# Kernel tuning notes

Hardware: AMD Instinct MI355X
Metric: run time of the kernel (lower is better)

## Reference

```python
import jax, jax.numpy as jnp
import numpy as np

B, L, C, S, W, R = 2, 32, 32, 64, 64, 32
MH = 32  # forcing MLP hidden


def _conv3d(x, w, b, pad_hw):
    # x: [B, Cin, L, S, W], w: [Cout, Cin, 1, kh, kw]
    y = jax.lax.conv_general_dilated(
        x, w, window_strides=(1, 1, 1),
        padding=[(0, 0), (pad_hw, pad_hw), (pad_hw, pad_hw)],
        dimension_numbers=('NCDHW', 'OIDHW', 'NCDHW'))
    return y + b[None, :, None, None, None]


def _forward(x, listT, params_log_base, dispersion_mod, fm_W1, fm_b1, fm_W2, fm_b2,
             forcing_scale, U_re, U_im, V_re, V_im, pW_re, pW_im, pb_re, pb_im,
             convr_w, convr_b, convi_w, convi_b, projc_w, projc_b, ln_w, ln_b):
    b, l, c, s, w = x.shape
    r = U_re.shape[-1]
    pad = s // 4
    dt = listT.reshape(b, l, 1, 1, 1)

    # FFT with mirror padding along S
    xp = jnp.pad(x, ((0, 0), (0, 0), (0, 0), (pad, pad), (0, 0)), mode='reflect')
    h = jnp.fft.fft2(xp.astype(jnp.complex64), axes=(-2, -1), norm='ortho')

    # complex channel projection
    proj_W = pW_re + 1j * pW_im
    h = jnp.einsum('blcsw,cd->bldsw', h, proj_W)
    h = h + (pb_re + 1j * pb_im)[None, None, :, None, None]

    # back to spatial, crop pad, re-FFT
    hs = jnp.fft.ifft2(h, axes=(-2, -1), norm='ortho')[..., pad:-pad, :]
    h = jnp.fft.fft2(hs, axes=(-2, -1), norm='ortho')

    U = U_re + 1j * U_im          # [C, S, R]
    V = V_re + 1j * V_im          # [C, W, R]
    # zq[b,l,c,r,q] = sum_{s,w} h * conj(U)[c,s,r] * V[c,w,q]
    zq = jnp.einsum('blcsw,csr,cwq->blcrq', h, jnp.conj(U), V)

    nu_base = jnp.exp(params_log_base[0] + dispersion_mod[0]).reshape(1, 1, c, r, 1)
    th_base = jnp.exp(params_log_base[1] + dispersion_mod[1]).reshape(1, 1, c, r, 1)

    # forcing modulation
    ctx = x.mean(axis=(-2, -1))                       # [B, L, C]
    inp = jnp.concatenate([ctx, dt.reshape(b, l, 1)], axis=-1)
    mid = jnp.tanh(inp @ fm_W1 + fm_b1)
    mod = (mid @ fm_W2 + fm_b2).reshape(b, l, c, r, 2)
    dnu = (forcing_scale * jnp.tanh(mod[..., 0]))[..., None]
    dth = (forcing_scale * jnp.tanh(mod[..., 1]))[..., None]

    nu_t = jnp.maximum(nu_base * dt + dnu, 1e-6)       # [B, L, C, R, 1]
    th_t = th_base * dt + dth
    lamb = jnp.exp(jax.lax.complex(-nu_t, th_t))       # complex [B, L, C, R, 1]

    gamma = jnp.sqrt(jnp.maximum(1.0 - jnp.exp(-2.0 * nu_t), 1e-12))
    x_in = zq * gamma.astype(zq.dtype)                 # [B, L, C, R, R]

    # parallel linear-recurrence scan: z_t = lamb_t * z_{t-1} + x_t
    def comb(a, bb):
        a1, x1 = a
        a2, x2 = bb
        return a1 * a2, a2 * x1 + x2
    _, z_out = jax.lax.associative_scan(comb, (lamb, x_in), axis=1)

    # reconstruct spectral field and inverse FFT
    h_rec = jnp.einsum('blcrq,cwq,csr->blcsw', z_out, jnp.conj(V), U)
    h_sp = jnp.fft.ifft2(h_rec, axes=(-2, -1), norm='ortho')

    xr = jnp.transpose(h_sp.real, (0, 2, 1, 3, 4))     # [B, C, L, S, W]
    xi = jnp.transpose(h_sp.imag, (0, 2, 1, 3, 4))
    hr = _conv3d(xr, convr_w, convr_b, 1)
    hi = _conv3d(xi, convi_w, convi_b, 1)
    hf = _conv3d(jnp.concatenate([hr, hi], axis=1), projc_w, projc_b, 0)
    hf = jnp.transpose(hf, (0, 2, 1, 3, 4))            # [B, L, C, S, W]

    # LayerNorm over [S, W]
    mu = hf.mean(axis=(-2, -1), keepdims=True)
    var = hf.var(axis=(-2, -1), keepdims=True)
    hf = (hf - mu) / jnp.sqrt(var + 1e-5) * ln_w + ln_b

    return x + hf


def setup_inputs() -> dict:
    key = jax.random.key(0)
    ks = jax.random.split(key, 20)
    f32 = jnp.float32
    x = jax.random.normal(ks[0], (B, L, C, S, W), dtype=f32)
    listT = jax.random.uniform(ks[1], (B, L), dtype=f32, minval=0.5, maxval=1.5)

    r_min, r_max = 0.8, 0.99
    u1 = jax.random.uniform(ks[2], (C, R), dtype=f32)
    u2 = jax.random.uniform(ks[3], (C, R), dtype=f32)
    nu_log = jnp.log(-0.5 * jnp.log(u1 * (r_max ** 2 - r_min ** 2) + r_min ** 2))
    theta_log = jnp.log(u2 * (2.0 * np.pi))
    params_log_base = jnp.stack([nu_log, theta_log], axis=0)
    dispersion_mod = jnp.zeros((2, C, R), dtype=f32)

    fm_W1 = jax.random.normal(ks[4], (C + 1, MH), dtype=f32) / np.sqrt(C + 1)
    fm_b1 = jnp.zeros((MH,), dtype=f32)
    fm_W2 = jax.random.normal(ks[5], (MH, C * R * 2), dtype=f32) / np.sqrt(MH)
    fm_b2 = jnp.zeros((C * R * 2,), dtype=f32)
    forcing_scale = jnp.float32(0.1)

    cplx_scale = 1.0 / np.sqrt(2.0)
    U_re = jax.random.normal(ks[6], (C, S, R), dtype=f32) * cplx_scale / np.sqrt(S)
    U_im = jax.random.normal(ks[7], (C, S, R), dtype=f32) * cplx_scale / np.sqrt(S)
    V_re = jax.random.normal(ks[8], (C, W, R), dtype=f32) * cplx_scale / np.sqrt(W)
    V_im = jax.random.normal(ks[9], (C, W, R), dtype=f32) * cplx_scale / np.sqrt(W)
    pW_re = jax.random.normal(ks[10], (C, C), dtype=f32) * cplx_scale / np.sqrt(C)
    pW_im = jax.random.normal(ks[11], (C, C), dtype=f32) * cplx_scale / np.sqrt(C)
    pb_re = jnp.zeros((C,), dtype=f32)
    pb_im = jnp.zeros((C,), dtype=f32)

    convr_w = jax.random.normal(ks[12], (C, C, 1, 3, 3), dtype=f32) * (1.0 / np.sqrt(C * 9))
    convr_b = jnp.zeros((C,), dtype=f32)
    convi_w = jax.random.normal(ks[13], (C, C, 1, 3, 3), dtype=f32) * (1.0 / np.sqrt(C * 9))
    convi_b = jnp.zeros((C,), dtype=f32)
    projc_w = jax.random.normal(ks[14], (C, 2 * C, 1, 1, 1), dtype=f32) * (1.0 / np.sqrt(2 * C))
    projc_b = jnp.zeros((C,), dtype=f32)

    ln_w = jnp.ones((S, W), dtype=f32)
    ln_b = jnp.zeros((S, W), dtype=f32)

    return dict(x=x, listT=listT, params_log_base=params_log_base,
                dispersion_mod=dispersion_mod, fm_W1=fm_W1, fm_b1=fm_b1,
                fm_W2=fm_W2, fm_b2=fm_b2, forcing_scale=forcing_scale,
                U_re=U_re, U_im=U_im, V_re=V_re, V_im=V_im,
                pW_re=pW_re, pW_im=pW_im, pb_re=pb_re, pb_im=pb_im,
                convr_w=convr_w, convr_b=convr_b, convi_w=convi_w, convi_b=convi_b,
                projc_w=projc_w, projc_b=projc_b, ln_w=ln_w, ln_b=ln_b)


def reference(x, listT, params_log_base, dispersion_mod, fm_W1, fm_b1, fm_W2, fm_b2,
              forcing_scale, U_re, U_im, V_re, V_im, pW_re, pW_im, pb_re, pb_im,
              convr_w, convr_b, convi_w, convi_b, projc_w, projc_b, ln_w, ln_b):
    return _forward(x, listT, params_log_base, dispersion_mod, fm_W1, fm_b1, fm_W2,
                    fm_b2, forcing_scale, U_re, U_im, V_re, V_im, pW_re, pW_im,
                    pb_re, pb_im, convr_w, convr_b, convi_w, convi_b, projc_w,
                    projc_b, ln_w, ln_b)
```

## Files before the change

kernel.cpp:

```cpp
#include <hip/hip_runtime.h>


typedef __attribute__((ext_vector_type(8))) short short8;
typedef __attribute__((ext_vector_type(4))) float floatx4;

__device__ __forceinline__ unsigned pack_bf16(float re, float im) {
  unsigned a = __float_as_uint(re), b = __float_as_uint(im);
  a = (a + 0x7FFFu + ((a >> 16) & 1u)) >> 16;
  b = (b + 0x7FFFu + ((b >> 16) & 1u)) >> 16;
  return a | (b << 16);
}
__device__ __forceinline__ unsigned short bf16r(float v) {
  unsigned a = __float_as_uint(v);
  return (unsigned short)((a + 0x7FFFu + ((a >> 16) & 1u)) >> 16);
}

__global__ __launch_bounds__(256) void k_mixprep(
    const float* __restrict__ x, const float* __restrict__ pWr,
    const float* __restrict__ pWi,
    const float* __restrict__ U_re, const float* __restrict__ U_im,
    const float* __restrict__ V_re, const float* __restrict__ V_im,
    const float* __restrict__ projc_w, const float* __restrict__ convr_w,
    const float* __restrict__ convi_w,
    const float* __restrict__ listT, const float* __restrict__ plb,
    const float* __restrict__ dmod, const float* __restrict__ W1,
    const float* __restrict__ b1, const float* __restrict__ W2,
    const float* __restrict__ b2, const float* __restrict__ fscale,
    unsigned* __restrict__ hs, unsigned* __restrict__ zqA,
    unsigned* __restrict__ recA, unsigned* __restrict__ recB,
    unsigned* __restrict__ Wtb, float2* __restrict__ lam,
    float* __restrict__ gam) {
  __shared__ __align__(16) char smem[33280];
  const int tid = threadIdx.x;
  const int bid = blockIdx.x;
  if (bid < 64) {
    float* cred = (float*)smem;
    float* ctxs = cred + 256;
    float* mid_s = ctxs + 32;
    const int bl = bid;
    {
      int c = tid >> 3, sub = tid & 7;
      const float4* xb = (const float4*)(x + (size_t)bl * 131072 + c * 4096);
      float s = 0.f;
#pragma unroll 8
      for (int m = 0; m < 128; ++m) {
        float4 v = xb[sub + m * 8];
        s += v.x + v.y + v.z + v.w;
      }
      cred[c * 8 + sub] = s;
    }
    __syncthreads();
    if (tid < 32) {
      float t = 0.f;
#pragma unroll
      for (int k = 0; k < 8; ++k) t += cred[tid * 8 + k];
      ctxs[tid] = t * (1.f / 4096.f);
    }
    __syncthreads();
    float dt = listT[bl];
    if (tid < 32) {
      float a = b1[tid];
      for (int j = 0; j < 32; ++j) a += ctxs[j] * W1[j * 32 + tid];
      a += dt * W1[1024 + tid];
      mid_s[tid] = tanhf(a);
    }
    __syncthreads();
    float fs = fscale[0];
#pragma unroll
    for (int u = 0; u < 4; ++u) {
      int cr = u * 256 + tid;
      int col = cr * 2;
      float m0 = b2[col], m1 = b2[col + 1];
      for (int h = 0; h < 32; ++h) {
        float mh = mid_s[h];
        float2 w2 = *(const float2*)&W2[h * 2048 + col];
        m0 += mh * w2.x;
        m1 += mh * w2.y;
      }
      float dnu = fs * tanhf(m0);
      float dth = fs * tanhf(m1);
      float nub = expf(plb[cr] + dmod[cr]);
      float thb = expf(plb[1024 + cr] + dmod[1024 + cr]);
      float nut = fmaxf(nub * dt + dnu, 1e-6f);
      float tht = thb * dt + dth;
      float e = expf(-nut);
      float sa, ca;
      sincosf(tht, &sa, &ca);
      float g = sqrtf(fmaxf(1.f - expf(-2.f * nut), 1e-12f));
      int o = bl * 1024 + cr;
      lam[o] = make_float2(e * ca, e * sa);
      gam[o] = g;
    }
  } else if (bid < 1088) {
    unsigned* xb_s = (unsigned*)smem;
    unsigned* outb = (unsigned*)smem;
    const int wk = bid - 64;
    const int bl = wk >> 4;
    const int seg = wk & 15;
    const int pxbase = seg * 256;
    const float* xb = x + (size_t)bl * 131072 + pxbase;
#pragma unroll
    for (int t = 0; t < 4; ++t) {
      int i = t * 256 + tid;
      int c2 = i & 15, g4 = i >> 4;
      float4 a = *(const float4*)(xb + (2 * c2) * 4096 + g4 * 4);
      float4 b = *(const float4*)(xb + (2 * c2 + 1) * 4096 + g4 * 4);
#pragma unroll
      for (int j = 0; j < 4; ++j) {
        int px = g4 * 4 + j;
        xb_s[px * 20 + (((c2 >> 2) ^ (px & 3)) << 2) + (c2 & 3)] =
            pack_bf16(((const float*)&a)[j], ((const float*)&b)[j]);
      }
    }
    const int lane = tid & 63, wv = tid >> 6;
    const int qd = lane >> 4, ln = lane & 15;
    short8 arL, aiL, arH, aiH;
#pragma unroll
    for (int j = 0; j < 8; ++j) {
      int ci = qd * 8 + j;
      ((short*)&arL)[j] = (short)bf16r(pWr[ci * 32 + ln]);
      ((short*)&aiL)[j] = (short)bf16r(pWi[ci * 32 + ln]);
      ((short*)&arH)[j] = (short)bf16r(pWr[ci * 32 + 16 + ln]);
      ((short*)&aiH)[j] = (short)bf16r(pWi[ci * 32 + 16 + ln]);
    }
    __syncthreads();
    floatx4 RL[4], IL[4], RH[4], IH[4];
#pragma unroll
    for (int pt = 0; pt < 4; ++pt) {
      int pxt = wv * 4 + pt;
      int pxl = pxt * 16 + ln;
      short8 bfr = *(const short8*)&xb_s[pxl * 20 + ((qd ^ (pxl & 3)) << 2)];
      floatx4 z4 = {0.f, 0.f, 0.f, 0.f};
      RL[pt] = __builtin_amdgcn_mfma_f32_16x16x32_bf16(arL, bfr, z4, 0, 0, 0);
      IL[pt] = __builtin_amdgcn_mfma_f32_16x16x32_bf16(aiL, bfr, z4, 0, 0, 0);
      RH[pt] = __builtin_amdgcn_mfma_f32_16x16x32_bf16(arH, bfr, z4, 0, 0, 0);
      IH[pt] = __builtin_amdgcn_mfma_f32_16x16x32_bf16(aiH, bfr, z4, 0, 0, 0);
    }
    __syncthreads();
#pragma unroll
    for (int pt = 0; pt < 4; ++pt) {
      int px = (wv * 4 + pt) * 16 + ln;
#pragma unroll
      for (int j = 0; j < 4; ++j) {
        outb[(qd * 4 + j) * 260 + px] = pack_bf16(RL[pt][j], IL[pt][j]);
        outb[(16 + qd * 4 + j) * 260 + px] = pack_bf16(RH[pt][j], IH[pt][j]);
      }
    }
    __syncthreads();
    unsigned* ho = hs + (size_t)bl * 131072 + pxbase;
    const int px4 = tid & 63, dg = tid >> 6;
#pragma unroll
    for (int dd = 0; dd < 8; ++dd) {
      int d = dg * 8 + dd;
      uint4 v = *(const uint4*)&outb[d * 260 + px4 * 4];
      *(uint4*)(ho + d * 4096 + px4 * 4) = v;
    }
  } else if (bid < 1152) {
    float2* A2 = (float2*)smem;
    float2* tw = (float2*)(smem + 16384);
    const int id = bid - 1088;
    const int c = id >> 1, src = id & 1;
    const float* Ar = (src ? V_re : U_re) + c * 2048;
    const float* Ai = (src ? V_im : U_im) + c * 2048;
    if (tid < 64) {
      float sa, ca;
      sincosf((float)tid * 0.09817477042468103f, &sa, &ca);
      tw[tid] = make_float2(ca, sa);
    }
#pragma unroll
    for (int t = 0; t < 8; ++t) {
      int idx = t * 256 + tid;
      A2[idx] = make_float2(Ar[idx], Ai[idx]);
    }
    __syncthreads();
    const int kw = tid >> 2, mg = tid & 3;
    float sr[8] = {0.f, 0.f, 0.f, 0.f, 0.f, 0.f, 0.f, 0.f};
    float si[8] = {0.f, 0.f, 0.f, 0.f, 0.f, 0.f, 0.f, 0.f};
#pragma unroll 4
    for (int n = 0; n < 64; ++n) {
      float2 w = tw[(kw * n) & 63];
      float ws = src ? -w.y : w.y;
#pragma unroll
      for (int t4 = 0; t4 < 4; ++t4) {
        float4 q = *(const float4*)&A2[n * 32 + mg * 8 + t4 * 2];
        sr[2 * t4]     += q.x * w.x - q.y * ws;
        si[2 * t4]     += q.x * ws + q.y * w.x;
        sr[2 * t4 + 1] += q.z * w.x - q.w * ws;
        si[2 * t4 + 1] += q.z * ws + q.w * w.x;
      }
    }
#pragma unroll
    for (int j = 0; j < 8; ++j) {
      float r = sr[j] * 0.125f, i2 = si[j] * 0.125f;
      int m = mg * 8 + j;
      unsigned p_ri  = pack_bf16(r, i2);
      unsigned p_rmi = pack_bf16(r, -i2);
      unsigned p_ir  = pack_bf16(i2, r);
      unsigned p_mir = pack_bf16(-i2, r);
      if (src == 0) {
        zqA[((c * 4 + 2) * 32 + m) * 64 + kw] = p_ri;
        zqA[((c * 4 + 3) * 32 + m) * 64 + kw] = p_mir;
        recA[((c * 2 + 0) * 64 + kw) * 32 + m] = p_rmi;
        recA[((c * 2 + 1) * 64 + kw) * 32 + m] = p_ir;
      } else {
        zqA[((c * 4 + 0) * 32 + m) * 64 + kw] = p_rmi;
        zqA[((c * 4 + 1) * 32 + m) * 64 + kw] = p_ir;
        recB[((c * 2 + 0) * 64 + kw) * 32 + m] = p_ri;
        recB[((c * 2 + 1) * 64 + kw) * 32 + m] = p_mir;
      }
    }
  } else {
    int gid = (bid - 1152) * 256 + tid;
    if (gid < 9216) {
      int co = gid / 288;
      int r2 = gid - co * 288;
      int tap = r2 >> 5, ci = r2 & 31;
      float sr = 0.f, si = 0.f;
      for (int m = 0; m < 32; ++m) {
        sr += projc_w[co * 64 + m]      * convr_w[(m * 32 + ci) * 9 + tap];
        si += projc_w[co * 64 + 32 + m] * convi_w[(m * 32 + ci) * 9 + tap];
      }
      Wtb[gid] = pack_bf16(sr, si);
    }
  }
}

__global__ __launch_bounds__(512, 2) void k_mid(
    const unsigned* __restrict__ hs, const short* __restrict__ zqA,
    const short* __restrict__ recA, const short* __restrict__ recB,
    const float2* __restrict__ lam, const float* __restrict__ gam,
    unsigned* __restrict__ hsp) {
  __shared__ __align__(16) char smem[61440];
  float2* lam_s = (float2*)smem;
  float*  gam_s = (float*)(smem + 8192);
  unsigned* HsB = (unsigned*)(smem + 12288);
  float2* zqt   = (float2*)(smem + 12288);
  unsigned* zB  = (unsigned*)(smem + 28672);
  unsigned* T2P = (unsigned*)(smem + 45056);
  const int tid = threadIdx.x;
  const int b = blockIdx.x >> 5, c = blockIdx.x & 31;
  const int lane = tid & 63, wv = tid >> 6;
  const int grp = wv >> 2, wvg = wv & 3;
  const int tg = tid & 255;
  const int qd = lane >> 4, ln = lane & 15;
  const int mt = wvg >> 1, nth = wvg & 1;
  const short* zA = zqA + (size_t)c * 4 * 32 * 128;
  short8 a1[4], a2[4], a3[4], a4[4];
#pragma unroll
  for (int t = 0; t < 4; ++t) {
    int row = mt * 16 + ln;
    a1[t] = *(const short8*)(zA + (0 * 32 + row) * 128 + t * 32 + qd * 8);
    a2[t] = *(const short8*)(zA + (1 * 32 + row) * 128 + t * 32 + qd * 8);
    a3[t] = *(const short8*)(zA + (2 * 32 + row) * 128 + t * 32 + qd * 8);
    a4[t] = *(const short8*)(zA + (3 * 32 + row) * 128 + t * 32 + qd * 8);
  }
  const short* rA = recA + (size_t)c * 2 * 64 * 64;
  short8 a5[2], a6[2];
#pragma unroll
  for (int t = 0; t < 2; ++t) {
    int row = wvg * 16 + ln;
    a5[t] = *(const short8*)(rA + (0 * 64 + row) * 64 + t * 32 + qd * 8);
    a6[t] = *(const short8*)(rA + (1 * 64 + row) * 64 + t * 32 + qd * 8);
  }
  const short* rB = recB + (size_t)c * 2 * 64 * 64;
  for (int idx = tid; idx < 1024; idx += 512) {
    int l = idx >> 5, r = idx & 31;
    lam_s[idx] = lam[(b * 32 + l) * 1024 + c * 32 + r];
    gam_s[idx] = gam[(b * 32 + l) * 1024 + c * 32 + r];
  }
  {
    const uint4* hp =
        (const uint4*)(hs + (size_t)((b * 32 + grp) * 32 + c) * 4096);
#pragma unroll
    for (int it = 0; it < 4; ++it) {
      int i4 = tg + it * 256;
      uint4 v = hp[i4];
      int s = i4 >> 4, w4 = i4 & 15;
      *(uint4*)&HsB[grp * 4096 + s * 64 + ((w4 ^ (s & 15)) << 2)] = v;
    }
  }
  float2 st[4];
#pragma unroll
  for (int j = 0; j < 4; ++j) st[j] = make_float2(0.f, 0.f);
  __syncthreads();
  for (int round = 0; round < 16; ++round) {
    const int l0 = round * 2;
    const int blc = (b * 32 + l0 + grp) * 32 + c;
#pragma unroll
    for (int nti = 0; nti < 2; ++nti) {
      int nt = nth * 2 + nti;
      int n = nt * 16 + ln;
      floatx4 accr = {0.f, 0.f, 0.f, 0.f}, acci = {0.f, 0.f, 0.f, 0.f};
#pragma unroll
      for (int t = 0; t < 4; ++t) {
        short8 bb = *(const short8*)&HsB[grp * 4096 + n * 64 +
                                         (((4 * t + qd) ^ (n & 15)) << 2)];
        accr = __builtin_amdgcn_mfma_f32_16x16x32_bf16(a1[t], bb, accr, 0, 0, 0);
        acci = __builtin_amdgcn_mfma_f32_16x16x32_bf16(a2[t], bb, acci, 0, 0, 0);
      }
#pragma unroll
      for (int j = 0; j < 4; ++j) {
        int q = mt * 16 + qd * 4 + j;
        int s = n;
        T2P[grp * 2048 + q * 64 + (((s >> 2) ^ (q & 15)) << 2) + (s & 3)] =
            pack_bf16(accr[j], acci[j]);
      }
    }
    __syncthreads();
    {
      int n = nth * 16 + ln;
      floatx4 zr = {0.f, 0.f, 0.f, 0.f}, zi = {0.f, 0.f, 0.f, 0.f};
#pragma unroll
      for (int t = 0; t < 4; ++t) {
        short8 bb = *(const short8*)&T2P[grp * 2048 + n * 64 +
                                         (((4 * t + qd) ^ (n & 15)) << 2)];
        zr = __builtin_amdgcn_mfma_f32_16x16x32_bf16(a3[t], bb, zr, 0, 0, 0);
        zi = __builtin_amdgcn_mfma_f32_16x16x32_bf16(a4[t], bb, zi, 0, 0, 0);
      }
#pragma unroll
      for (int j = 0; j < 4; ++j) {
        int r = mt * 16 + qd * 4 + j;
        zqt[grp * 1024 + r * 32 + n] = make_float2(zr[j], zi[j]);
      }
    }
    __syncthreads();
    {
      int q = nth * 16 + ln;
#pragma unroll
      for (int j = 0; j < 4; ++j) {
        int r = mt * 16 + qd * 4 + j;
        float2 lm = lam_s[l0 * 32 + r];
        float g = gam_s[l0 * 32 + r];
        float2 v = zqt[r * 32 + q];
        float nr = lm.x * st[j].x - lm.y * st[j].y + g * v.x;
        float ni = lm.x * st[j].y + lm.y * st[j].x + g * v.y;
        st[j] = make_float2(nr, ni);
        unsigned pk = pack_bf16(nr, ni);
        lm = lam_s[(l0 + 1) * 32 + r];
        g = gam_s[(l0 + 1) * 32 + r];
        v = zqt[1024 + r * 32 + q];
        nr = lm.x * st[j].x - lm.y * st[j].y + g * v.x;
        ni = lm.x * st[j].y + lm.y * st[j].x + g * v.y;
        st[j] = make_float2(nr, ni);
        if (grp) pk = pack_bf16(nr, ni);
        zB[grp * 1024 + q * 32 + (((r >> 2) ^ (q & 7)) << 2) + (r & 3)] = pk;
      }
    }
    __syncthreads();
#pragma unroll
    for (int nt = 0; nt < 2; ++nt) {
      int n = nt * 16 + ln;
      floatx4 pr = {0.f, 0.f, 0.f, 0.f}, pi = {0.f, 0.f, 0.f, 0.f};
#pragma unroll
      for (int t = 0; t < 2; ++t) {
        short8 bb = *(const short8*)&zB[grp * 1024 + n * 32 +
                                        (((4 * t + qd) ^ (n & 7)) << 2)];
        pr = __builtin_amdgcn_mfma_f32_16x16x32_bf16(a5[t], bb, pr, 0, 0, 0);
        pi = __builtin_amdgcn_mfma_f32_16x16x32_bf16(a6[t], bb, pi, 0, 0, 0);
      }
#pragma unroll
      for (int j = 0; j < 4; ++j) {
        int s = wvg * 16 + qd * 4 + j;
        int q = n;
        T2P[grp * 2048 + s * 32 + (((q >> 2) ^ (s & 7)) << 2) + (q & 3)] =
            pack_bf16(pr[j], pi[j]);
      }
    }
    __syncthreads();
    uint4 sv[4];
    const bool more = (round < 15);
    if (more) {
      const uint4* hp = (const uint4*)(
          hs + (size_t)((b * 32 + l0 + 2 + grp) * 32 + c) * 4096);
#pragma unroll
      for (int it = 0; it < 4; ++it) sv[it] = hp[tg + it * 256];
    }
    {
      short8 pa[2];
      int row = wvg * 16 + ln;
#pragma unroll
      for (int t = 0; t < 2; ++t)
        pa[t] = *(const short8*)&T2P[grp * 2048 + row * 32 +
                                     (((4 * t + qd) ^ (row & 7)) << 2)];
      unsigned* ho = hsp + (size_t)blc * 4096;
#pragma unroll
      for (int nt = 0; nt < 4; ++nt) {
        int n = nt * 16 + ln;
        floatx4 hr = {0.f, 0.f, 0.f, 0.f}, hi = {0.f, 0.f, 0.f, 0.f};
#pragma unroll
        for (int t = 0; t < 2; ++t) {
          short8 b5 = *(const short8*)(rB + (0 * 64 + n) * 64 + t * 32 + qd * 8);
          short8 b6 = *(const short8*)(rB + (1 * 64 + n) * 64 + t * 32 + qd * 8);
          hr = __builtin_amdgcn_mfma_f32_16x16x32_bf16(pa[t], b5, hr, 0, 0, 0);
          hi = __builtin_amdgcn_mfma_f32_16x16x32_bf16(pa[t], b6, hi, 0, 0, 0);
        }
#pragma unroll
        for (int j = 0; j < 4; ++j) {
          int s = wvg * 16 + qd * 4 + j;
          ho[s * 64 + n] = pack_bf16(hr[j], hi[j]);
        }
      }
    }
    if (more) {
#pragma unroll
      for (int it = 0; it < 4; ++it) {
        int i4 = tg + it * 256;
        int s = i4 >> 4, w4 = i4 & 15;
        *(uint4*)&HsB[grp * 4096 + s * 64 + ((w4 ^ (s & 15)) << 2)] = sv[it];
      }
    }
    __syncthreads();
  }
}

__global__ __launch_bounds__(256, 2) void k_conv(
    const unsigned* __restrict__ hsp, const short* __restrict__ Wtb,
    unsigned short* __restrict__ convout, float2* __restrict__ stats) {
  __shared__ unsigned lds_in[6 * 66 * 32];
  const int bl = blockIdx.x >> 4;
  const int slab = blockIdx.x & 15;
  const int y0 = slab * 4;
  const int tid = threadIdx.x;
  for (int i = tid; i < 384; i += 256) {
    int ci = i & 31, j = i >> 5;
    int yi = j >> 1, xi = (j & 1) ? 65 : 0;
    int slot = (ci >> 2) ^ (xi & 7);
    lds_in[(yi * 66 + xi) * 32 + slot * 4 + (ci & 3)] = 0u;
  }
#pragma unroll
  for (int t = 0; t < 12; ++t) {
    int i = t * 256 + tid;
    int ci = i & 31;
    int j = i >> 5;
    int yi = j >> 4, x4 = j & 15;
    int y = y0 + yi - 1;
    uint4 v = make_uint4(0u, 0u, 0u, 0u);
    if ((unsigned)y < 64u)
      v = *(const uint4*)(hsp + (((size_t)bl * 32 + ci) * 64 + y) * 64 + x4 * 4);
    int xb = 1 + x4 * 4;
#pragma unroll
    for (int jj = 0; jj < 4; ++jj) {
      int xi = xb + jj;
      int slot = (ci >> 2) ^ (xi & 7);
      lds_in[(yi * 66 + xi) * 32 + slot * 4 + (ci & 3)] =
          ((const unsigned*)&v)[jj];
    }
  }
  const int lane = tid & 63;
  const int wv = tid >> 6;
  const int co = lane & 15;
  const int qd = lane >> 4;
  short8 bL[18], bH[18];
  {
    const short* wpL = Wtb + (co * 9) * 64 + qd * 8;
    const short* wpH = Wtb + ((co + 16) * 9) * 64 + qd * 8;
#pragma unroll
    for (int tap = 0; tap < 9; ++tap)
#pragma unroll
      for (int kk = 0; kk < 2; ++kk) {
        bL[tap * 2 + kk] = *(const short8*)(wpL + tap * 64 + kk * 32);
        bH[tap * 2 + kk] = *(const short8*)(wpH + tap * 64 + kk * 32);
      }
  }
  __syncthreads();
  float sL = 0.f, s2L = 0.f, sH = 0.f, s2H = 0.f;
  const int x0 = wv * 16;
  const int xl = lane & 15;
  for (int ry = 0; ry < 4; ++ry) {
    floatx4 aL = {0.f, 0.f, 0.f, 0.f}, aH = {0.f, 0.f, 0.f, 0.f};
#pragma unroll
    for (int tap = 0; tap < 9; ++tap) {
      int dy = tap / 3, dx = tap - dy * 3;
      int yi = ry + dy;
      int xi = x0 + xl + dx;
#pragma unroll
      for (int kk = 0; kk < 2; ++kk) {
        int slot = ((kk << 2) | qd) ^ (xi & 7);
        const short8 a =
            *(const short8*)&lds_in[(yi * 66 + xi) * 32 + slot * 4];
        aL = __builtin_amdgcn_mfma_f32_16x16x32_bf16(a, bL[tap * 2 + kk], aL, 0, 0, 0);
        aH = __builtin_amdgcn_mfma_f32_16x16x32_bf16(a, bH[tap * 2 + kk], aH, 0, 0, 0);
      }
    }
    size_t goL = (((size_t)bl * 32 + co) * 64 + (y0 + ry)) * 64 + x0 + qd * 4;
    size_t goH = goL + (size_t)16 * 4096;
    *(uint2*)(convout + goL) =
        make_uint2(pack_bf16(aL[0], aL[1]), pack_bf16(aL[2], aL[3]));
    *(uint2*)(convout + goH) =
        make_uint2(pack_bf16(aH[0], aH[1]), pack_bf16(aH[2], aH[3]));
#pragma unroll
    for (int j = 0; j < 4; ++j) {
      sL += aL[j]; s2L += aL[j] * aL[j];
      sH += aH[j]; s2H += aH[j] * aH[j];
    }
  }
  sL += __shfl_down(sL, 32, 64);  s2L += __shfl_down(s2L, 32, 64);
  sH += __shfl_down(sH, 32, 64);  s2H += __shfl_down(s2H, 32, 64);
  sL += __shfl_down(sL, 16, 64);  s2L += __shfl_down(s2L, 16, 64);
  sH += __shfl_down(sH, 16, 64);  s2H += __shfl_down(s2H, 16, 64);
  if (lane < 16) {
    stats[((size_t)bl * 32 + lane) * 64 + slab * 4 + wv] = make_float2(sL, s2L);
    stats[((size_t)bl * 32 + 16 + lane) * 64 + slab * 4 + wv] =
        make_float2(sH, s2H);
  }
}

__global__ __launch_bounds__(256) void k_ln(
    const unsigned short* __restrict__ convout,
    const float2* __restrict__ stats, const float* __restrict__ x,
    const float* __restrict__ ln_w, const float* __restrict__ ln_b,
    float* __restrict__ out) {
  const int blc = blockIdx.x;
  const int tid = threadIdx.x;
  __shared__ float sh_mu, sh_rs;
  if (tid < 64) {
    float2 v = stats[(size_t)blc * 64 + tid];
    float s = v.x, s2 = v.y;
#pragma unroll
    for (int o = 32; o > 0; o >>= 1) {
      s += __shfl_down(s, o, 64);
      s2 += __shfl_down(s2, o, 64);
    }
    if (tid == 0) {
      float mu = s * (1.f / 4096.f);
      float var = s2 * (1.f / 4096.f) - mu * mu;
      sh_mu = mu;
      sh_rs = rsqrtf(var + 1e-5f);
    }
  }
  __syncthreads();
  float mu = sh_mu, rs = sh_rs;
  const uint2* cp = (const uint2*)(convout + (size_t)blc * 4096);
  const float4* xp = (const float4*)(x + (size_t)blc * 4096);
  const float4* lwp = (const float4*)ln_w;
  const float4* lbp = (const float4*)ln_b;
  float4* op = (float4*)(out + (size_t)blc * 4096);
#pragma unroll
  for (int k = 0; k < 4; ++k) {
    int i = tid + k * 256;
    uint2 cv = cp[i];
    float4 xv = xp[i], lw = lwp[i], lb = lbp[i];
    float c0 = __uint_as_float(cv.x << 16);
    float c1 = __uint_as_float(cv.x & 0xFFFF0000u);
    float c2 = __uint_as_float(cv.y << 16);
    float c3 = __uint_as_float(cv.y & 0xFFFF0000u);
    float4 o;
    o.x = xv.x + (c0 - mu) * rs * lw.x + lb.x;
    o.y = xv.y + (c1 - mu) * rs * lw.y + lb.y;
    o.z = xv.z + (c2 - mu) * rs * lw.z + lb.z;
    o.w = xv.w + (c3 - mu) * rs * lw.w + lb.w;
    op[i] = o;
  }
}

extern "C" void kernel_launch(void* const* d_in, const int* in_sizes, int n_in,
                              void* d_out, int out_size, void* d_ws,
                              size_t ws_size, hipStream_t stream) {
  const float* x       = (const float*)d_in[0];
  const float* listT   = (const float*)d_in[1];
  const float* plb     = (const float*)d_in[2];
  const float* dmod    = (const float*)d_in[3];
  const float* fm_W1   = (const float*)d_in[4];
  const float* fm_b1   = (const float*)d_in[5];
  const float* fm_W2   = (const float*)d_in[6];
  const float* fm_b2   = (const float*)d_in[7];
  const float* fscale  = (const float*)d_in[8];
  const float* U_re    = (const float*)d_in[9];
  const float* U_im    = (const float*)d_in[10];
  const float* V_re    = (const float*)d_in[11];
  const float* V_im    = (const float*)d_in[12];
  const float* pW_re   = (const float*)d_in[13];
  const float* pW_im   = (const float*)d_in[14];
  const float* convr_w = (const float*)d_in[17];
  const float* convi_w = (const float*)d_in[19];
  const float* projc_w = (const float*)d_in[21];
  const float* ln_w    = (const float*)d_in[23];
  const float* ln_b    = (const float*)d_in[24];
  float* out = (float*)d_out;

  float* wsf = (float*)d_ws;
  unsigned* hs   = (unsigned*)wsf;
  unsigned* hsp  = (unsigned*)(wsf + 8388608);
  unsigned* zqAp = (unsigned*)(wsf + 16777216);
  unsigned* recAp = (unsigned*)(wsf + 17039360);
  unsigned* recBp = (unsigned*)(wsf + 17170432);
  unsigned short* convout = (unsigned short*)(wsf + 17301504);
  float2*   stats = (float2*)(wsf + 25690112);
  float2*   lam   = (float2*)(wsf + 25952256);
  float*    gam   = wsf + 26083328;
  unsigned* Wtb   = (unsigned*)(wsf + 26148864);

  k_mixprep<<<1188, 256, 0, stream>>>(x, pW_re, pW_im, U_re, U_im, V_re, V_im,
                                      projc_w, convr_w, convi_w, listT, plb,
                                      dmod, fm_W1, fm_b1, fm_W2, fm_b2, fscale,
                                      hs, zqAp, recAp, recBp, Wtb, lam, gam);
  k_mid<<<64, 512, 0, stream>>>(hs, (const short*)zqAp, (const short*)recAp,
                                (const short*)recBp, lam, gam, hsp);
  k_conv<<<1024, 256, 0, stream>>>(hsp, (const short*)Wtb, convout, stats);
  k_ln<<<2048, 256, 0, stream>>>(convout, stats, x, ln_w, ln_b, out);
}
```

Before: 264.7 us.

## Split sequential scan across L-segments with decoupled lookback carry propagation

The recurrent mid kernel previously ran 64 blocks, each scanning all 32 time steps serially. It now launches 256 blocks, each handling an 8-step segment. Each block computes a local scan, then receives its carry from the previous segment through a flag-and-buffer chain in global memory and applies the decayed carry before the output projections. The forcing-MLP and lambda/gamma computation moves into this kernel, using per-segment channel sums that the mix kernel now produces as a side output. This removes the separate context-reduction blocks. The intent is much better GPU occupancy on the latency-bound recurrence, at the cost of a spin-wait dependency chain and a memset that rely on all blocks being co-resident.

```diff
diff --git a/kernel.cpp b/kernel.cpp
--- a/kernel.cpp
+++ b/kernel.cpp
@@ -22,89 +22,28 @@
     const float* __restrict__ V_re, const float* __restrict__ V_im,
     const float* __restrict__ projc_w, const float* __restrict__ convr_w,
     const float* __restrict__ convi_w,
-    const float* __restrict__ listT, const float* __restrict__ plb,
-    const float* __restrict__ dmod, const float* __restrict__ W1,
-    const float* __restrict__ b1, const float* __restrict__ W2,
-    const float* __restrict__ b2, const float* __restrict__ fscale,
-    unsigned* __restrict__ hs, unsigned* __restrict__ zqA,
-    unsigned* __restrict__ recA, unsigned* __restrict__ recB,
-    unsigned* __restrict__ Wtb, float2* __restrict__ lam,
-    float* __restrict__ gam) {
+    unsigned* __restrict__ hs, float* __restrict__ ctxp,
+    unsigned* __restrict__ zqA, unsigned* __restrict__ recA,
+    unsigned* __restrict__ recB, unsigned* __restrict__ Wtb) {
   __shared__ __align__(16) char smem[33280];
   const int tid = threadIdx.x;
-  const int bid = blockIdx.x;
-  if (bid < 64) {
-    float* cred = (float*)smem;
-    float* ctxs = cred + 256;
-    float* mid_s = ctxs + 32;
-    const int bl = bid;
-    {
-      int c = tid >> 3, sub = tid & 7;
-      const float4* xb = (const float4*)(x + (size_t)bl * 131072 + c * 4096);
-      float s = 0.f;
-#pragma unroll 8
-      for (int m = 0; m < 128; ++m) {
-        float4 v = xb[sub + m * 8];
-        s += v.x + v.y + v.z + v.w;
-      }
-      cred[c * 8 + sub] = s;
-    }
-    __syncthreads();
-    if (tid < 32) {
-      float t = 0.f;
-#pragma unroll
-      for (int k = 0; k < 8; ++k) t += cred[tid * 8 + k];
-      ctxs[tid] = t * (1.f / 4096.f);
-    }
-    __syncthreads();
-    float dt = listT[bl];
-    if (tid < 32) {
-      float a = b1[tid];
-      for (int j = 0; j < 32; ++j) a += ctxs[j] * W1[j * 32 + tid];
-      a += dt * W1[1024 + tid];
-      mid_s[tid] = tanhf(a);
-    }
-    __syncthreads();
-    float fs = fscale[0];
-#pragma unroll
-    for (int u = 0; u < 4; ++u) {
-      int cr = u * 256 + tid;
-      int col = cr * 2;
-      float m0 = b2[col], m1 = b2[col + 1];
-      for (int h = 0; h < 32; ++h) {
-        float mh = mid_s[h];
-        float2 w2 = *(const float2*)&W2[h * 2048 + col];
-        m0 += mh * w2.x;
-        m1 += mh * w2.y;
-      }
-      float dnu = fs * tanhf(m0);
-      float dth = fs * tanhf(m1);
-      float nub = expf(plb[cr] + dmod[cr]);
-      float thb = expf(plb[1024 + cr] + dmod[1024 + cr]);
-      float nut = fmaxf(nub * dt + dnu, 1e-6f);
-      float tht = thb * dt + dth;
-      float e = expf(-nut);
-      float sa, ca;
-      sincosf(tht, &sa, &ca);
-      float g = sqrtf(fmaxf(1.f - expf(-2.f * nut), 1e-12f));
-      int o = bl * 1024 + cr;
-      lam[o] = make_float2(e * ca, e * sa);
-      gam[o] = g;
-    }
-  } else if (bid < 1088) {
+  if (blockIdx.x < 1024) {
     unsigned* xb_s = (unsigned*)smem;
+    float(*red)[16][2] = (float(*)[16][2])(smem + 20480);
     unsigned* outb = (unsigned*)smem;
-    const int wk = bid - 64;
-    const int bl = wk >> 4;
-    const int seg = wk & 15;
+    const int bl = blockIdx.x >> 4;
+    const int seg = blockIdx.x & 15;
     const int pxbase = seg * 256;
     const float* xb = x + (size_t)bl * 131072 + pxbase;
+    float csa = 0.f, csb = 0.f;
 #pragma unroll
     for (int t = 0; t < 4; ++t) {
       int i = t * 256 + tid;
       int c2 = i & 15, g4 = i >> 4;
       float4 a = *(const float4*)(xb + (2 * c2) * 4096 + g4 * 4);
       float4 b = *(const float4*)(xb + (2 * c2 + 1) * 4096 + g4 * 4);
+      csa += a.x + a.y + a.z + a.w;
+      csb += b.x + b.y + b.z + b.w;
 #pragma unroll
       for (int j = 0; j < 4; ++j) {
         int px = g4 * 4 + j;
@@ -112,6 +51,8 @@
             pack_bf16(((const float*)&a)[j], ((const float*)&b)[j]);
       }
     }
+    red[tid & 15][tid >> 4][0] = csa;
+    red[tid & 15][tid >> 4][1] = csb;
     const int lane = tid & 63, wv = tid >> 6;
     const int qd = lane >> 4, ln = lane & 15;
     short8 arL, aiL, arH, aiH;
@@ -124,6 +65,13 @@
       ((short*)&aiH)[j] = (short)bf16r(pWi[ci * 32 + 16 + ln]);
     }
     __syncthreads();
+    if (tid < 32) {
+      int c2 = tid >> 1, part = tid & 1;
+      float s = 0.f;
+#pragma unroll
+      for (int w = 0; w < 16; ++w) s += red[c2][w][part];
+      ctxp[(bl * 16 + seg) * 32 + 2 * c2 + part] = s;
+    }
     floatx4 RL[4], IL[4], RH[4], IH[4];
 #pragma unroll
     for (int pt = 0; pt < 4; ++pt) {
@@ -155,10 +103,10 @@
       uint4 v = *(const uint4*)&outb[d * 260 + px4 * 4];
       *(uint4*)(ho + d * 4096 + px4 * 4) = v;
     }
-  } else if (bid < 1152) {
+  } else if (blockIdx.x < 1088) {
     float2* A2 = (float2*)smem;
     float2* tw = (float2*)(smem + 16384);
-    const int id = bid - 1088;
+    const int id = blockIdx.x - 1024;
     const int c = id >> 1, src = id & 1;
     const float* Ar = (src ? V_re : U_re) + c * 2048;
     const float* Ai = (src ? V_im : U_im) + c * 2048;
@@ -210,7 +158,7 @@
       }
     }
   } else {
-    int gid = (bid - 1152) * 256 + tid;
+    int gid = (blockIdx.x - 1088) * 256 + tid;
     if (gid < 9216) {
       int co = gid / 288;
       int r2 = gid - co * 288;
@@ -225,25 +173,65 @@
   }
 }
 
-__global__ __launch_bounds__(512, 2) void k_mid(
+__global__ __launch_bounds__(256) void k_mid2(
     const unsigned* __restrict__ hs, const short* __restrict__ zqA,
     const short* __restrict__ recA, const short* __restrict__ recB,
-    const float2* __restrict__ lam, const float* __restrict__ gam,
-    unsigned* __restrict__ hsp) {
-  __shared__ __align__(16) char smem[61440];
-  float2* lam_s = (float2*)smem;
-  float*  gam_s = (float*)(smem + 8192);
-  unsigned* HsB = (unsigned*)(smem + 12288);
-  float2* zqt   = (float2*)(smem + 12288);
-  unsigned* zB  = (unsigned*)(smem + 28672);
-  unsigned* T2P = (unsigned*)(smem + 45056);
+    const float* __restrict__ ctxp, const float* __restrict__ listT,
+    const float* __restrict__ plb, const float* __restrict__ dmod,
+    const float* __restrict__ W1, const float* __restrict__ b1,
+    const float* __restrict__ W2, const float* __restrict__ b2,
+    const float* __restrict__ fscale, unsigned* __restrict__ hsp,
+    unsigned long long* __restrict__ cbuf, int* __restrict__ cflag) {
+  __shared__ __align__(16) unsigned HsB[4096];
+  __shared__ __align__(16) unsigned T2[2048];
+  __shared__ unsigned zB[1024];
+  __shared__ float2 lam_s[8][32];
+  __shared__ float gam_s[8][32];
+  __shared__ float ctxs[8][32], mids[8][32];
   const int tid = threadIdx.x;
-  const int b = blockIdx.x >> 5, c = blockIdx.x & 31;
+  const int bcs = blockIdx.x;
+  const int seg = bcs & 3, bc = bcs >> 2;
+  const int b = bc >> 5, c = bc & 31;
+  const int l0g = seg * 8;
+  {
+    const int g = tid >> 5, t = tid & 31;
+    const int bl = b * 32 + l0g + g;
+    float s = 0.f;
+#pragma unroll
+    for (int sg = 0; sg < 16; ++sg) s += ctxp[(bl * 16 + sg) * 32 + t];
+    ctxs[g][t] = s * (1.f / 4096.f);
+    __syncthreads();
+    float a = b1[t];
+    for (int j = 0; j < 32; ++j) a += ctxs[g][j] * W1[j * 32 + t];
+    const float dt = listT[bl];
+    a += dt * W1[1024 + t];
+    mids[g][t] = tanhf(a);
+    __syncthreads();
+    const int cr = c * 32 + t;
+    const int col = cr * 2;
+    float m0 = b2[col], m1 = b2[col + 1];
+    for (int h = 0; h < 32; ++h) {
+      float mh = mids[g][h];
+      float2 w2 = *(const float2*)&W2[h * 2048 + col];
+      m0 += mh * w2.x;
+      m1 += mh * w2.y;
+    }
+    const float fs = fscale[0];
+    float dnu = fs * tanhf(m0);
+    float dth = fs * tanhf(m1);
+    float nub = expf(plb[cr] + dmod[cr]);
+    float thb = expf(plb[1024 + cr] + dmod[1024 + cr]);
+    float nut = fmaxf(nub * dt + dnu, 1e-6f);
+    float tht = thb * dt + dth;
+    float e = expf(-nut);
+    float sa, ca;
+    sincosf(tht, &sa, &ca);
+    lam_s[g][t] = make_float2(e * ca, e * sa);
+    gam_s[g][t] = sqrtf(fmaxf(1.f - expf(-2.f * nut), 1e-12f));
+  }
   const int lane = tid & 63, wv = tid >> 6;
-  const int grp = wv >> 2, wvg = wv & 3;
-  const int tg = tid & 255;
   const int qd = lane >> 4, ln = lane & 15;
-  const int mt = wvg >> 1, nth = wvg & 1;
+  const int mt = wv >> 1, nth = wv & 1;
   const short* zA = zqA + (size_t)c * 4 * 32 * 128;
   short8 a1[4], a2[4], a3[4], a4[4];
 #pragma unroll
@@ -258,34 +246,36 @@
   short8 a5[2], a6[2];
 #pragma unroll
   for (int t = 0; t < 2; ++t) {
-    int row = wvg * 16 + ln;
+    int row = wv * 16 + ln;
     a5[t] = *(const short8*)(rA + (0 * 64 + row) * 64 + t * 32 + qd * 8);
     a6[t] = *(const short8*)(rA + (1 * 64 + row) * 64 + t * 32 + qd * 8);
   }
   const short* rB = recB + (size_t)c * 2 * 64 * 64;
-  for (int idx = tid; idx < 1024; idx += 512) {
-    int l = idx >> 5, r = idx & 31;
-    lam_s[idx] = lam[(b * 32 + l) * 1024 + c * 32 + r];
-    gam_s[idx] = gam[(b * 32 + l) * 1024 + c * 32 + r];
-  }
   {
     const uint4* hp =
-        (const uint4*)(hs + (size_t)((b * 32 + grp) * 32 + c) * 4096);
+        (const uint4*)(hs + (size_t)((b * 32 + l0g) * 32 + c) * 4096);
 #pragma unroll
     for (int it = 0; it < 4; ++it) {
-      int i4 = tg + it * 256;
+      int i4 = tid + it * 256;
       uint4 v = hp[i4];
       int s = i4 >> 4, w4 = i4 & 15;
-      *(uint4*)&HsB[grp * 4096 + s * 64 + ((w4 ^ (s & 15)) << 2)] = v;
-    }
-  }
-  float2 st[4];
+      *(uint4*)&HsB[s * 64 + ((w4 ^ (s & 15)) << 2)] = v;
+    }
+  }
+  float2 st[4], zloc[8][4];
 #pragma unroll
   for (int j = 0; j < 4; ++j) st[j] = make_float2(0.f, 0.f);
+  const int q = nth * 16 + ln;
   __syncthreads();
-  for (int round = 0; round < 16; ++round) {
-    const int l0 = round * 2;
-    const int blc = (b * 32 + l0 + grp) * 32 + c;
+#pragma unroll
+  for (int l = 0; l < 8; ++l) {
+    uint4 sv[4];
+    if (l < 7) {
+      const uint4* hp = (const uint4*)(
+          hs + (size_t)((b * 32 + l0g + l + 1) * 32 + c) * 4096);
+#pragma unroll
+      for (int it = 0; it < 4; ++it) sv[it] = hp[tid + it * 256];
+    }
 #pragma unroll
     for (int nti = 0; nti < 2; ++nti) {
       int nt = nth * 2 + nti;
@@ -293,58 +283,113 @@
       floatx4 accr = {0.f, 0.f, 0.f, 0.f}, acci = {0.f, 0.f, 0.f, 0.f};
 #pragma unroll
       for (int t = 0; t < 4; ++t) {
-        short8 bb = *(const short8*)&HsB[grp * 4096 + n * 64 +
-                                         (((4 * t + qd) ^ (n & 15)) << 2)];
+        short8 bb =
+            *(const short8*)&HsB[n * 64 + (((4 * t + qd) ^ (n & 15)) << 2)];
         accr = __builtin_amdgcn_mfma_f32_16x16x32_bf16(a1[t], bb, accr, 0, 0, 0);
         acci = __builtin_amdgcn_mfma_f32_16x16x32_bf16(a2[t], bb, acci, 0, 0, 0);
       }
 #pragma unroll
       for (int j = 0; j < 4; ++j) {
-        int q = mt * 16 + qd * 4 + j;
+        int qq = mt * 16 + qd * 4 + j;
         int s = n;
-        T2P[grp * 2048 + q * 64 + (((s >> 2) ^ (q & 15)) << 2) + (s & 3)] =
+        T2[qq * 64 + (((s >> 2) ^ (qq & 15)) << 2) + (s & 3)] =
             pack_bf16(accr[j], acci[j]);
       }
     }
     __syncthreads();
     {
-      int n = nth * 16 + ln;
       floatx4 zr = {0.f, 0.f, 0.f, 0.f}, zi = {0.f, 0.f, 0.f, 0.f};
 #pragma unroll
       for (int t = 0; t < 4; ++t) {
-        short8 bb = *(const short8*)&T2P[grp * 2048 + n * 64 +
-                                         (((4 * t + qd) ^ (n & 15)) << 2)];
+        short8 bb =
+            *(const short8*)&T2[q * 64 + (((4 * t + qd) ^ (q & 15)) << 2)];
         zr = __builtin_amdgcn_mfma_f32_16x16x32_bf16(a3[t], bb, zr, 0, 0, 0);
         zi = __builtin_amdgcn_mfma_f32_16x16x32_bf16(a4[t], bb, zi, 0, 0, 0);
       }
 #pragma unroll
       for (int j = 0; j < 4; ++j) {
         int r = mt * 16 + qd * 4 + j;
-        zqt[grp * 1024 + r * 32 + n] = make_float2(zr[j], zi[j]);
-      }
-    }
-    __syncthreads();
-    {
-      int q = nth * 16 + ln;
-#pragma unroll
-      for (int j = 0; j < 4; ++j) {
-        int r = mt * 16 + qd * 4 + j;
-        float2 lm = lam_s[l0 * 32 + r];
-        float g = gam_s[l0 * 32 + r];
-        float2 v = zqt[r * 32 + q];
-        float nr = lm.x * st[j].x - lm.y * st[j].y + g * v.x;
-        float ni = lm.x * st[j].y + lm.y * st[j].x + g * v.y;
+        float2 lm = lam_s[l][r];
+        float g = gam_s[l][r];
+        float nr = lm.x * st[j].x - lm.y * st[j].y + g * zr[j];
+        float ni = lm.x * st[j].y + lm.y * st[j].x + g * zi[j];
         st[j] = make_float2(nr, ni);
-        unsigned pk = pack_bf16(nr, ni);
-        lm = lam_s[(l0 + 1) * 32 + r];
-        g = gam_s[(l0 + 1) * 32 + r];
-        v = zqt[1024 + r * 32 + q];
-        nr = lm.x * st[j].x - lm.y * st[j].y + g * v.x;
-        ni = lm.x * st[j].y + lm.y * st[j].x + g * v.y;
-        st[j] = make_float2(nr, ni);
-        if (grp) pk = pack_bf16(nr, ni);
-        zB[grp * 1024 + q * 32 + (((r >> 2) ^ (q & 7)) << 2) + (r & 3)] = pk;
-      }
+        zloc[l][j] = st[j];
+      }
+    }
+    if (l < 7) {
+#pragma unroll
+      for (int it = 0; it < 4; ++it) {
+        int i4 = tid + it * 256;
+        int s = i4 >> 4, w4 = i4 & 15;
+        *(uint4*)&HsB[s * 64 + ((w4 ^ (s & 15)) << 2)] = sv[it];
+      }
+    }
+    __syncthreads();
+  }
+  float2 carry[4];
+#pragma unroll
+  for (int j = 0; j < 4; ++j) carry[j] = make_float2(0.f, 0.f);
+  if (seg > 0) {
+    if (tid == 0) {
+      while (__hip_atomic_load(&cflag[bcs - 1], __ATOMIC_ACQUIRE,
+                               __HIP_MEMORY_SCOPE_AGENT) == 0)
+        __builtin_amdgcn_s_sleep(2);
+    }
+    __syncthreads();
+#pragma unroll
+    for (int j = 0; j < 4; ++j) {
+      int r = mt * 16 + qd * 4 + j;
+      unsigned long long v =
+          __hip_atomic_load(&cbuf[(size_t)(bcs - 1) * 1024 + r * 32 + q],
+                            __ATOMIC_RELAXED, __HIP_MEMORY_SCOPE_AGENT);
+      carry[j] = make_float2(__uint_as_float((unsigned)v),
+                             __uint_as_float((unsigned)(v >> 32)));
+    }
+  }
+  if (seg < 3) {
+#pragma unroll
+    for (int j = 0; j < 4; ++j) {
+      int r = mt * 16 + qd * 4 + j;
+      float2 pp = make_float2(1.f, 0.f);
+#pragma unroll
+      for (int l = 0; l < 8; ++l) {
+        float2 lm = lam_s[l][r];
+        float nr = pp.x * lm.x - pp.y * lm.y;
+        float ni = pp.x * lm.y + pp.y * lm.x;
+        pp = make_float2(nr, ni);
+      }
+      float2 inc;
+      inc.x = st[j].x + pp.x * carry[j].x - pp.y * carry[j].y;
+      inc.y = st[j].y + pp.x * carry[j].y + pp.y * carry[j].x;
+      unsigned long long v =
+          (unsigned long long)__float_as_uint(inc.x) |
+          ((unsigned long long)__float_as_uint(inc.y) << 32);
+      __hip_atomic_store(&cbuf[(size_t)bcs * 1024 + r * 32 + q], v,
+                         __ATOMIC_RELAXED, __HIP_MEMORY_SCOPE_AGENT);
+    }
+    __threadfence();
+    __syncthreads();
+    if (tid == 0)
+      __hip_atomic_store(&cflag[bcs], 1, __ATOMIC_RELEASE,
+                         __HIP_MEMORY_SCOPE_AGENT);
+  }
+  float2 d[4];
+#pragma unroll
+  for (int j = 0; j < 4; ++j) d[j] = carry[j];
+#pragma unroll
+  for (int l = 0; l < 8; ++l) {
+    const int blc = (b * 32 + l0g + l) * 32 + c;
+#pragma unroll
+    for (int j = 0; j < 4; ++j) {
+      int r = mt * 16 + qd * 4 + j;
+      float2 lm = lam_s[l][r];
+      float nr = d[j].x * lm.x - d[j].y * lm.y;
+      float ni = d[j].x * lm.y + d[j].y * lm.x;
+      d[j] = make_float2(nr, ni);
+      float zx = zloc[l][j].x + d[j].x;
+      float zy = zloc[l][j].y + d[j].y;
+      zB[q * 32 + (((r >> 2) ^ (q & 7)) << 2) + (r & 3)] = pack_bf16(zx, zy);
     }
     __syncthreads();
 #pragma unroll
@@ -353,35 +398,27 @@
       floatx4 pr = {0.f, 0.f, 0.f, 0.f}, pi = {0.f, 0.f, 0.f, 0.f};
 #pragma unroll
       for (int t = 0; t < 2; ++t) {
-        short8 bb = *(const short8*)&zB[grp * 1024 + n * 32 +
-                                        (((4 * t + qd) ^ (n & 7)) << 2)];
+        short8 bb =
+            *(const short8*)&zB[n * 32 + (((4 * t + qd) ^ (n & 7)) << 2)];
         pr = __builtin_amdgcn_mfma_f32_16x16x32_bf16(a5[t], bb, pr, 0, 0, 0);
         pi = __builtin_amdgcn_mfma_f32_16x16x32_bf16(a6[t], bb, pi, 0, 0, 0);
       }
 #pragma unroll
       for (int j = 0; j < 4; ++j) {
-        int s = wvg * 16 + qd * 4 + j;
-        int q = n;
-        T2P[grp * 2048 + s * 32 + (((q >> 2) ^ (s & 7)) << 2) + (q & 3)] =
+        int s = wv * 16 + qd * 4 + j;
+        int qq = n;
+        T2[s * 32 + (((qq >> 2) ^ (s & 7)) << 2) + (qq & 3)] =
             pack_bf16(pr[j], pi[j]);
       }
     }
     __syncthreads();
-    uint4 sv[4];
-    const bool more = (round < 15);
-    if (more) {
-      const uint4* hp = (const uint4*)(
-          hs + (size_t)((b * 32 + l0 + 2 + grp) * 32 + c) * 4096);
-#pragma unroll
-      for (int it = 0; it < 4; ++it) sv[it] = hp[tg + it * 256];
-    }
     {
       short8 pa[2];
-      int row = wvg * 16 + ln;
+      int row = wv * 16 + ln;
 #pragma unroll
       for (int t = 0; t < 2; ++t)
-        pa[t] = *(const short8*)&T2P[grp * 2048 + row * 32 +
-                                     (((4 * t + qd) ^ (row & 7)) << 2)];
+        pa[t] = *(const short8*)&T2[row * 32 +
+                                    (((4 * t + qd) ^ (row & 7)) << 2)];
       unsigned* ho = hsp + (size_t)blc * 4096;
 #pragma unroll
       for (int nt = 0; nt < 4; ++nt) {
@@ -396,17 +433,9 @@
         }
 #pragma unroll
         for (int j = 0; j < 4; ++j) {
-          int s = wvg * 16 + qd * 4 + j;
+          int s = wv * 16 + qd * 4 + j;
           ho[s * 64 + n] = pack_bf16(hr[j], hi[j]);
         }
-      }
-    }
-    if (more) {
-#pragma unroll
-      for (int it = 0; it < 4; ++it) {
-        int i4 = tg + it * 256;
-        int s = i4 >> 4, w4 = i4 & 15;
-        *(uint4*)&HsB[grp * 4096 + s * 64 + ((w4 ^ (s & 15)) << 2)] = sv[it];
       }
     }
     __syncthreads();
@@ -585,17 +614,21 @@
   unsigned* recAp = (unsigned*)(wsf + 17039360);
   unsigned* recBp = (unsigned*)(wsf + 17170432);
   unsigned short* convout = (unsigned short*)(wsf + 17301504);
-  float2*   stats = (float2*)(wsf + 25690112);
-  float2*   lam   = (float2*)(wsf + 25952256);
-  float*    gam   = wsf + 26083328;
-  unsigned* Wtb   = (unsigned*)(wsf + 26148864);
-
-  k_mixprep<<<1188, 256, 0, stream>>>(x, pW_re, pW_im, U_re, U_im, V_re, V_im,
-                                      projc_w, convr_w, convi_w, listT, plb,
-                                      dmod, fm_W1, fm_b1, fm_W2, fm_b2, fscale,
-                                      hs, zqAp, recAp, recBp, Wtb, lam, gam);
-  k_mid<<<64, 512, 0, stream>>>(hs, (const short*)zqAp, (const short*)recAp,
-                                (const short*)recBp, lam, gam, hsp);
+  float2*   stats = (float2*)(wsf + 21495808);
+  unsigned* Wtb   = (unsigned*)(wsf + 21757952);
+  float*    ctxp  = wsf + 21767168;
+  unsigned long long* cbuf =
+      (unsigned long long*)(wsf + 21799936);
+  int*      cflag = (int*)(wsf + 22324224);
+
+  hipMemsetAsync(cflag, 0, 1024, stream);
+  k_mixprep<<<1124, 256, 0, stream>>>(x, pW_re, pW_im, U_re, U_im, V_re, V_im,
+                                      projc_w, convr_w, convi_w, hs, ctxp,
+                                      zqAp, recAp, recBp, Wtb);
+  k_mid2<<<256, 256, 0, stream>>>(hs, (const short*)zqAp, (const short*)recAp,
+                                  (const short*)recBp, ctxp, listT, plb, dmod,
+                                  fm_W1, fm_b1, fm_W2, fm_b2, fscale, hsp,
+                                  cbuf, cflag);
   k_conv<<<1024, 256, 0, stream>>>(hsp, (const short*)Wtb, convout, stats);
   k_ln<<<2048, 256, 0, stream>>>(convout, stats, x, ln_w, ln_b, out);
 }
```

Result: slower. 302.5 us (+14.3%).
